# Optimization experiments

Measured on AMD Instinct MI355X. Metric: run time of the kernel, lower is better.

## Reference

```python
import jax, jax.numpy as jnp
import numpy as np

B, IN, H, OUT, E = 8192, 1024, 4096, 1024, 8
HG = H // 2  # gating hidden

def setup_inputs() -> dict:
    key = jax.random.key(0)
    ks = jax.random.split(key, 9)
    s_in = 1.0 / np.sqrt(IN)
    s_h = 1.0 / np.sqrt(H)
    s_hg = 1.0 / np.sqrt(HG)
    return {
        "x": jax.random.normal(ks[0], (B, IN), jnp.float32),
        # gating MLP: Linear(IN,HG) -> ReLU -> Linear(HG,E) -> softmax
        "gw1": jax.random.uniform(ks[1], (IN, HG), jnp.float32, -s_in, s_in),
        "gb1": jax.random.uniform(ks[2], (HG,), jnp.float32, -s_in, s_in),
        "gw2": jax.random.uniform(ks[3], (HG, E), jnp.float32, -s_hg, s_hg),
        "gb2": jax.random.uniform(ks[4], (E,), jnp.float32, -s_hg, s_hg),
        # experts: E x (Linear(IN,H) -> ReLU -> Linear(H,OUT))
        "ew1": jax.random.uniform(ks[5], (E, IN, H), jnp.float32, -s_in, s_in),
        "eb1": jax.random.uniform(ks[6], (E, H), jnp.float32, -s_in, s_in),
        "ew2": jax.random.uniform(ks[7], (E, H, OUT), jnp.float32, -s_h, s_h),
        "eb2": jax.random.uniform(ks[8], (E, OUT), jnp.float32, -s_h, s_h),
    }

def reference(x, gw1, gb1, gw2, gb2, ew1, eb1, ew2, eb2):
    # Gating network (dropout is a no-op in eval)
    gh = jax.nn.relu(x @ gw1 + gb1)                       # [B, HG]
    gates = jax.nn.softmax(gh @ gw2 + gb2, axis=1)        # [B, E]
    # All experts run on the full batch
    h = jax.nn.relu(jnp.einsum('bi,eih->beh', x, ew1) + eb1[None])  # [B, E, H]
    eo = jnp.einsum('beh,eho->beo', h, ew2) + eb2[None]             # [B, E, OUT]
    # Gate-weighted combine: (stacked * gates[...,None]).sum(dim=1)
    combined = jnp.einsum('beo,be->bo', eo, gates)        # [B, OUT]
    return combined
```

## Files before the change

### kernel.cpp

```cpp
#include <hip/hip_runtime.h>


#define DI __device__ __forceinline__

typedef _Float16 f16;
typedef _Float16 f16x8 __attribute__((ext_vector_type(8)));
typedef float f32x4 __attribute__((ext_vector_type(4)));

constexpr int BSZ  = 8192;
constexpr int IND  = 1024;
constexpr int HID  = 4096;
constexpr int OUTD = 1024;
constexpr int NE   = 8;
constexpr int HGD  = 2048;

__global__ __launch_bounds__(256) void conv_f32_f16_kernel(
    const float* __restrict__ in, f16* __restrict__ out)
{
    size_t i = ((size_t)blockIdx.x * 256 + threadIdx.x) * 8;
    const float4* p = (const float4*)(in + i);
    float4 a = p[0], b = p[1];
    f16x8 v = {(f16)a.x, (f16)a.y, (f16)a.z, (f16)a.w,
               (f16)b.x, (f16)b.y, (f16)b.z, (f16)b.w};
    *(f16x8*)(out + i) = v;
}

__global__ __launch_bounds__(256) void transpose_f32_f16_kernel(
    const float* __restrict__ W, f16* __restrict__ Wt, int K, int N)
{
    __shared__ float t[64][65];
    int n0 = blockIdx.x * 64, k0 = blockIdx.y * 64;
    int tx = threadIdx.x & 63, ty = threadIdx.x >> 6;
#pragma unroll
    for (int i = 0; i < 16; i++) {
        int k = i * 4 + ty;
        t[k][tx] = W[(size_t)(k0 + k) * N + n0 + tx];
    }
    __syncthreads();
#pragma unroll
    for (int i = 0; i < 16; i++) {
        int n = i * 4 + ty;
        Wt[(size_t)(n0 + n) * K + k0 + tx] = (f16)t[tx][n];
    }
}

DI void gload_lds16(const void* g, void* l)
{
    typedef const __attribute__((address_space(1))) unsigned int as1_t;
    typedef __attribute__((address_space(3))) unsigned int as3_t;
    __builtin_amdgcn_global_load_lds(
        (as1_t*)(unsigned long long)(__SIZE_TYPE__)g,
        (as3_t*)(unsigned int)(__SIZE_TYPE__)l,
        16, 0, 0);
}

template <bool RELU, bool GATE, bool OUT_F16, bool ACCUM>
__global__ __launch_bounds__(256, 2) void gemm_f16_kernel(
    const f16* __restrict__ A, const f16* __restrict__ Bt,
    const float* __restrict__ bias, const float* __restrict__ gate,
    void* __restrict__ Cptr, int M, int N, int K)
{
    constexpr int BK = 64;
    __shared__ __align__(16) f16 sA[128 * BK];
    __shared__ __align__(16) f16 sB[128 * BK];
    const int tid  = threadIdx.x;
    const int wid  = tid >> 6, lane = tid & 63;
    const size_t bm = (size_t)blockIdx.y * 128;
    const size_t bn = (size_t)blockIdx.x * 128;

    f32x4 acc[4][4] = {};

    int rr[4], oo[4];
#pragma unroll
    for (int i = 0; i < 4; i++) {
        int c = wid * 4 + i;
        rr[i] = c * 8 + (lane >> 3);
        oo[i] = ((((lane & 7) * 16) ^ ((rr[i] & 7) << 4)) >> 1);
    }
    const f16* Abase = A + bm * (size_t)K;
    const f16* Bbase = Bt + bn * (size_t)K;

    for (int kt = 0; kt < K; kt += BK) {
        __syncthreads();
#pragma unroll
        for (int i = 0; i < 4; i++) {
            int c = wid * 4 + i;
            gload_lds16(Abase + (size_t)rr[i] * K + kt + oo[i], (char*)sA + c * 1024);
            gload_lds16(Bbase + (size_t)rr[i] * K + kt + oo[i], (char*)sB + c * 1024);
        }
        __syncthreads();

#pragma unroll
        for (int kk = 0; kk < BK; kk += 32) {
            f16x8 av[4], bv[4];
            const int kb = (kk + ((lane >> 4) * 8)) * 2;
#pragma unroll
            for (int f = 0; f < 4; f++) {
                int Ra = ((wid >> 1) * 64) + f * 16 + (lane & 15);
                int Rb = ((wid & 1) * 64) + f * 16 + (lane & 15);
                av[f] = *(const f16x8*)((const char*)sA + Ra * 128 + (kb ^ ((Ra & 7) << 4)));
                bv[f] = *(const f16x8*)((const char*)sB + Rb * 128 + (kb ^ ((Rb & 7) << 4)));
            }
#pragma unroll
            for (int fm = 0; fm < 4; fm++)
#pragma unroll
                for (int fn = 0; fn < 4; fn++)
                    acc[fm][fn] = __builtin_amdgcn_mfma_f32_16x16x32_f16(
                        av[fm], bv[fn], acc[fm][fn], 0, 0, 0);
        }
    }

    const int wm = (wid >> 1) * 64, wn = (wid & 1) * 64;
    const int c0 = lane & 15, r0 = (lane >> 4) * 4;
#pragma unroll
    for (int fm = 0; fm < 4; fm++) {
#pragma unroll
        for (int r = 0; r < 4; r++) {
            const size_t row = bm + wm + fm * 16 + r0 + r;
            float g = 1.0f;
            if constexpr (GATE) g = gate[row * NE];
#pragma unroll
            for (int fn = 0; fn < 4; fn++) {
                const size_t col = bn + wn + fn * 16 + c0;
                float v = acc[fm][fn][r] + bias[col];
                if constexpr (RELU) v = fmaxf(v, 0.0f);
                if constexpr (GATE) v *= g;
                if constexpr (OUT_F16) {
                    ((f16*)Cptr)[row * (size_t)N + col] = (f16)v;
                } else {
                    float* p = (float*)Cptr + row * (size_t)N + col;
                    *p = ACCUM ? (*p + v) : v;
                }
            }
        }
    }
}

__global__ __launch_bounds__(256) void gate_softmax_kernel(
    const f16* __restrict__ gh, const float* __restrict__ gw2,
    const float* __restrict__ gb2, float* __restrict__ gates)
{
    const int row  = blockIdx.x * 4 + (threadIdx.x >> 6);
    const int lane = threadIdx.x & 63;
    const f16* r = gh + (size_t)row * HGD;
    float acc[NE] = {};
    for (int k = lane; k < HGD; k += 64) {
        float h = (float)r[k];
        const float* w = gw2 + (size_t)k * NE;
#pragma unroll
        for (int e = 0; e < NE; e++) acc[e] = fmaf(h, w[e], acc[e]);
    }
#pragma unroll
    for (int off = 32; off > 0; off >>= 1)
#pragma unroll
        for (int e = 0; e < NE; e++) acc[e] += __shfl_down(acc[e], off, 64);
    if (lane == 0) {
        float l[NE], m = -1e30f;
#pragma unroll
        for (int e = 0; e < NE; e++) { l[e] = acc[e] + gb2[e]; m = fmaxf(m, l[e]); }
        float s = 0.f;
#pragma unroll
        for (int e = 0; e < NE; e++) { l[e] = expf(l[e] - m); s += l[e]; }
        float inv = 1.0f / s;
#pragma unroll
        for (int e = 0; e < NE; e++) gates[(size_t)row * NE + e] = l[e] * inv;
    }
}

extern "C" void kernel_launch(void* const* d_in, const int* in_sizes, int n_in,
                              void* d_out, int out_size, void* d_ws, size_t ws_size,
                              hipStream_t stream)
{
    const float* x   = (const float*)d_in[0];
    const float* gw1 = (const float*)d_in[1];
    const float* gb1 = (const float*)d_in[2];
    const float* gw2 = (const float*)d_in[3];
    const float* gb2 = (const float*)d_in[4];
    const float* ew1 = (const float*)d_in[5];
    const float* eb1 = (const float*)d_in[6];
    const float* ew2 = (const float*)d_in[7];
    const float* eb2 = (const float*)d_in[8];
    float* out = (float*)d_out;

    char* ws = (char*)d_ws;
    float* gates = (float*)ws;
    f16* x16  = (f16*)(ws + (256 << 10));
    f16* wbuf = x16 + (size_t)BSZ * IND;
    f16* hbuf = wbuf + (size_t)HID * IND;
    f16* gh   = hbuf;

    conv_f32_f16_kernel<<<(BSZ * IND) / (256 * 8), 256, 0, stream>>>(x, x16);

    transpose_f32_f16_kernel<<<dim3(HGD / 64, IND / 64), 256, 0, stream>>>(gw1, wbuf, IND, HGD);
    gemm_f16_kernel<true, false, true, false>
        <<<dim3(HGD / 128, BSZ / 128), 256, 0, stream>>>(
            x16, wbuf, gb1, nullptr, gh, BSZ, HGD, IND);

    gate_softmax_kernel<<<BSZ / 4, 256, 0, stream>>>(gh, gw2, gb2, gates);

    for (int e = 0; e < NE; e++) {
        transpose_f32_f16_kernel<<<dim3(HID / 64, IND / 64), 256, 0, stream>>>(
            ew1 + (size_t)e * IND * HID, wbuf, IND, HID);
        gemm_f16_kernel<true, false, true, false>
            <<<dim3(HID / 128, BSZ / 128), 256, 0, stream>>>(
                x16, wbuf, eb1 + (size_t)e * HID, nullptr, hbuf, BSZ, HID, IND);

        transpose_f32_f16_kernel<<<dim3(OUTD / 64, HID / 64), 256, 0, stream>>>(
            ew2 + (size_t)e * HID * OUTD, wbuf, HID, OUTD);
        if (e == 0)
            gemm_f16_kernel<false, true, false, false>
                <<<dim3(OUTD / 128, BSZ / 128), 256, 0, stream>>>(
                    hbuf, wbuf, eb2 + (size_t)e * OUTD, gates + e, out, BSZ, OUTD, HID);
        else
            gemm_f16_kernel<false, true, false, true>
                <<<dim3(OUTD / 128, BSZ / 128), 256, 0, stream>>>(
                    hbuf, wbuf, eb2 + (size_t)e * OUTD, gates + e, out, BSZ, OUTD, HID);
    }
}
```

Baseline: 1.489 ms.

## Replace GEMM with 8-wave double-buffered ping-pong pipelined kernel using larger tiles

Replaces the simple 128x128 single-buffered f16 MFMA GEMM with a 512-thread kernel that uses 256xBN tiles, double-buffered LDS, B fragments held in registers, and explicit phase scheduling. Global-to-LDS loads for the next tile are interleaved with MFMA phases using barriers, waitcnt, and setprio. Workgroup IDs are remapped in an XCD-aware way. The goal is to hide memory latency and raise MFMA utilization, at the cost of much higher register and LDS pressure and fragile hand-tuned synchronization.

```diff
diff --git a/kernel.cpp b/kernel.cpp
--- a/kernel.cpp
+++ b/kernel.cpp
@@ -54,75 +54,141 @@
         16, 0, 0);
 }
 
-template <bool RELU, bool GATE, bool OUT_F16, bool ACCUM>
-__global__ __launch_bounds__(256, 2) void gemm_f16_kernel(
+
+#define PH(BUF, MH, KS, PRE, STAGE, VM)                                        \
+  {                                                                            \
+    f16x8 av0 = ldA(BUF, 0, MH, KS);                                           \
+    f16x8 av1 = ldA(BUF, 1, MH, KS);                                           \
+    f16x8 av2 = ldA(BUF, 2, MH, KS);                                           \
+    f16x8 av3 = ldA(BUF, 3, MH, KS);                                           \
+    if constexpr ((PRE) >= 0) {                                                \
+      _Pragma("unroll")                                                        \
+      for (int n = 0; n < NF; n++) breg[n][KS] = ldB(BUF, n, KS);              \
+    }                                                                          \
+    STAGE                                                                      \
+    __builtin_amdgcn_sched_barrier(0);                                         \
+    __builtin_amdgcn_s_barrier();                                              \
+    asm volatile("s_waitcnt lgkmcnt(0)" ::: "memory");                         \
+    __builtin_amdgcn_sched_barrier(0);                                         \
+    __builtin_amdgcn_s_setprio(1);                                             \
+    _Pragma("unroll")                                                          \
+    for (int n = 0; n < NF; n++) {                                             \
+      acc[(MH)*4+0][n] = __builtin_amdgcn_mfma_f32_16x16x32_f16(av0, breg[n][KS], acc[(MH)*4+0][n], 0, 0, 0); \
+      acc[(MH)*4+1][n] = __builtin_amdgcn_mfma_f32_16x16x32_f16(av1, breg[n][KS], acc[(MH)*4+1][n], 0, 0, 0); \
+      acc[(MH)*4+2][n] = __builtin_amdgcn_mfma_f32_16x16x32_f16(av2, breg[n][KS], acc[(MH)*4+2][n], 0, 0, 0); \
+      acc[(MH)*4+3][n] = __builtin_amdgcn_mfma_f32_16x16x32_f16(av3, breg[n][KS], acc[(MH)*4+3][n], 0, 0, 0); \
+    }                                                                          \
+    __builtin_amdgcn_s_setprio(0);                                             \
+    VM                                                                         \
+    __builtin_amdgcn_sched_barrier(0);                                         \
+    __builtin_amdgcn_s_barrier();                                              \
+    asm volatile("" ::: "memory");                                             \
+  }
+
+#define VMSTEP                                                                 \
+  { if (i + 1 == NI) { asm volatile("s_waitcnt vmcnt(0)"); }                   \
+    else if constexpr (BN == 256) { asm volatile("s_waitcnt vmcnt(4)"); }      \
+    else { asm volatile("s_waitcnt vmcnt(2)"); } }
+
+template <int BN, bool RELU, bool GATE, bool OUT_F16, bool ACCUM>
+__global__ __launch_bounds__(512, 2) void gemm8p_kernel(
     const f16* __restrict__ A, const f16* __restrict__ Bt,
     const float* __restrict__ bias, const float* __restrict__ gate,
     void* __restrict__ Cptr, int M, int N, int K)
 {
-    constexpr int BK = 64;
-    __shared__ __align__(16) f16 sA[128 * BK];
-    __shared__ __align__(16) f16 sB[128 * BK];
-    const int tid  = threadIdx.x;
-    const int wid  = tid >> 6, lane = tid & 63;
-    const size_t bm = (size_t)blockIdx.y * 128;
-    const size_t bn = (size_t)blockIdx.x * 128;
-
-    f32x4 acc[4][4] = {};
-
-    int rr[4], oo[4];
-#pragma unroll
-    for (int i = 0; i < 4; i++) {
-        int c = wid * 4 + i;
-        rr[i] = c * 8 + (lane >> 3);
-        oo[i] = ((((lane & 7) * 16) ^ ((rr[i] & 7) << 4)) >> 1);
-    }
-    const f16* Abase = A + bm * (size_t)K;
-    const f16* Bbase = Bt + bn * (size_t)K;
-
-    for (int kt = 0; kt < K; kt += BK) {
-        __syncthreads();
-#pragma unroll
-        for (int i = 0; i < 4; i++) {
-            int c = wid * 4 + i;
-            gload_lds16(Abase + (size_t)rr[i] * K + kt + oo[i], (char*)sA + c * 1024);
-            gload_lds16(Bbase + (size_t)rr[i] * K + kt + oo[i], (char*)sB + c * 1024);
-        }
-        __syncthreads();
-
-#pragma unroll
-        for (int kk = 0; kk < BK; kk += 32) {
-            f16x8 av[4], bv[4];
-            const int kb = (kk + ((lane >> 4) * 8)) * 2;
-#pragma unroll
-            for (int f = 0; f < 4; f++) {
-                int Ra = ((wid >> 1) * 64) + f * 16 + (lane & 15);
-                int Rb = ((wid & 1) * 64) + f * 16 + (lane & 15);
-                av[f] = *(const f16x8*)((const char*)sA + Ra * 128 + (kb ^ ((Ra & 7) << 4)));
-                bv[f] = *(const f16x8*)((const char*)sB + Rb * 128 + (kb ^ ((Rb & 7) << 4)));
-            }
-#pragma unroll
-            for (int fm = 0; fm < 4; fm++)
-#pragma unroll
-                for (int fn = 0; fn < 4; fn++)
-                    acc[fm][fn] = __builtin_amdgcn_mfma_f32_16x16x32_f16(
-                        av[fm], bv[fn], acc[fm][fn], 0, 0, 0);
-        }
-    }
-
-    const int wm = (wid >> 1) * 64, wn = (wid & 1) * 64;
+    constexpr int BM = 256, BK = 64;
+    constexpr int NF  = BN / 64;
+    constexpr int NBC = (BN * BK * 2) / 8192;
+    __shared__ __align__(16) f16 sA[2][BM * BK];
+    __shared__ __align__(16) f16 sB[2][BN * BK];
+
+    const int tid = threadIdx.x, wid = tid >> 6, lane = tid & 63;
+    const int wm = wid >> 2, wn = wid & 3;
+
+    const int nwg = gridDim.x;
+    const int bid = blockIdx.x;
+    const int wg  = (bid & 7) * (nwg >> 3) + (bid >> 3);
+    const int gx  = N / BN;
+    const size_t bm = (size_t)(wg / gx) * BM;
+    const size_t bn = (size_t)(wg % gx) * BN;
+
+    f32x4 acc[8][NF] = {};
+    f16x8 breg[NF][2];
+
+    const int srow = (wid << 3) + (lane >> 3);
+    const int scol = ((((lane & 7) << 4) ^ (((lane >> 3) & 7) << 4)) >> 1);
+    const f16* Ab = A  + (bm + srow) * (size_t)K + scol;
+    const f16* Bb = Bt + (bn + srow) * (size_t)K + scol;
+    char* sAb = (char*)&sA[0][0] + wid * 1024;
+    char* sBb = (char*)&sB[0][0] + wid * 1024;
+
+    auto stA = [&](int b, int q, int t) {
+        gload_lds16(Ab + (size_t)q * 64 * K + t * BK,
+                    sAb + b * (BM * BK * 2) + q * 8192);
+    };
+    auto stB = [&](int b, int q, int t) {
+        gload_lds16(Bb + (size_t)q * 64 * K + t * BK,
+                    sBb + b * (BN * BK * 2) + q * 8192);
+    };
+    auto ldA = [&](int b, int f, int mh, int ks) -> f16x8 {
+        int r  = wm * 128 + mh * 64 + f * 16 + (lane & 15);
+        int kb = (((ks * 32) + ((lane >> 4) << 3)) << 1) ^ ((r & 7) << 4);
+        return *(const f16x8*)((const char*)&sA[b][0] + r * 128 + kb);
+    };
+    auto ldB = [&](int b, int n, int ks) -> f16x8 {
+        int r  = wn * (BN / 4) + n * 16 + (lane & 15);
+        int kb = (((ks * 32) + ((lane >> 4) << 3)) << 1) ^ ((r & 7) << 4);
+        return *(const f16x8*)((const char*)&sB[b][0] + r * 128 + kb);
+    };
+
+    const int NT = K / BK, NI = NT / 2;
+
+#pragma unroll
+    for (int q = 0; q < 4; q++) stA(0, q, 0);
+#pragma unroll
+    for (int q = 0; q < NBC; q++) stB(0, q, 0);
+#pragma unroll
+    for (int q = 0; q < NBC; q++) stB(1, q, 1);
+    if constexpr (NBC == 4) { asm volatile("s_waitcnt vmcnt(4)"); }
+    else                    { asm volatile("s_waitcnt vmcnt(2)"); }
+    __builtin_amdgcn_s_barrier();
+    asm volatile("" ::: "memory");
+
+    for (int i = 0; i < NI; ++i) {
+        const int t = 2 * i;
+        const bool pf = (i + 1 < NI);
+        PH(0, 0, 0, 0,
+           { stA(1,0,t+1); stA(1,1,t+1); stA(1,2,t+1); stA(1,3,t+1); }, {})
+        PH(0, 0, 1, 1, {}, {})
+        PH(0, 1, 0, -1,
+           { if (pf) { stB(0,0,t+2); stB(0,1,t+2); } }, {})
+        PH(0, 1, 1, -1,
+           { if (pf) { if constexpr (NBC == 4) { stB(0,2,t+2); stB(0,3,t+2); } } },
+           VMSTEP)
+        PH(1, 0, 0, 0,
+           { if (pf) { stA(0,0,t+2); stA(0,1,t+2); stA(0,2,t+2); stA(0,3,t+2); } }, {})
+        PH(1, 0, 1, 1, {}, {})
+        PH(1, 1, 0, -1,
+           { if (pf) { stB(1,0,t+3); stB(1,1,t+3); } }, {})
+        PH(1, 1, 1, -1,
+           { if (pf) { if constexpr (NBC == 4) { stB(1,2,t+3); stB(1,3,t+3); } } },
+           VMSTEP)
+    }
+
+    const size_t row0 = bm + (size_t)wm * 128;
+    const int col0 = (int)bn + wn * (BN / 4);
     const int c0 = lane & 15, r0 = (lane >> 4) * 4;
 #pragma unroll
-    for (int fm = 0; fm < 4; fm++) {
+    for (int fm = 0; fm < 8; fm++) {
 #pragma unroll
         for (int r = 0; r < 4; r++) {
-            const size_t row = bm + wm + fm * 16 + r0 + r;
+            const size_t row = row0 + fm * 16 + r0 + r;
             float g = 1.0f;
             if constexpr (GATE) g = gate[row * NE];
 #pragma unroll
-            for (int fn = 0; fn < 4; fn++) {
-                const size_t col = bn + wn + fn * 16 + c0;
-                float v = acc[fm][fn][r] + bias[col];
+            for (int n = 0; n < NF; n++) {
+                const size_t col = (size_t)col0 + n * 16 + c0;
+                float v = acc[fm][n][r] + bias[col];
                 if constexpr (RELU) v = fmaxf(v, 0.0f);
                 if constexpr (GATE) v *= g;
                 if constexpr (OUT_F16) {
@@ -192,8 +258,8 @@
     conv_f32_f16_kernel<<<(BSZ * IND) / (256 * 8), 256, 0, stream>>>(x, x16);
 
     transpose_f32_f16_kernel<<<dim3(HGD / 64, IND / 64), 256, 0, stream>>>(gw1, wbuf, IND, HGD);
-    gemm_f16_kernel<true, false, true, false>
-        <<<dim3(HGD / 128, BSZ / 128), 256, 0, stream>>>(
+    gemm8p_kernel<256, true, false, true, false>
+        <<<(HGD / 256) * (BSZ / 256), 512, 0, stream>>>(
             x16, wbuf, gb1, nullptr, gh, BSZ, HGD, IND);
 
     gate_softmax_kernel<<<BSZ / 4, 256, 0, stream>>>(gh, gw2, gb2, gates);
@@ -201,19 +267,19 @@
     for (int e = 0; e < NE; e++) {
         transpose_f32_f16_kernel<<<dim3(HID / 64, IND / 64), 256, 0, stream>>>(
             ew1 + (size_t)e * IND * HID, wbuf, IND, HID);
-        gemm_f16_kernel<true, false, true, false>
-            <<<dim3(HID / 128, BSZ / 128), 256, 0, stream>>>(
+        gemm8p_kernel<256, true, false, true, false>
+            <<<(HID / 256) * (BSZ / 256), 512, 0, stream>>>(
                 x16, wbuf, eb1 + (size_t)e * HID, nullptr, hbuf, BSZ, HID, IND);
 
         transpose_f32_f16_kernel<<<dim3(OUTD / 64, HID / 64), 256, 0, stream>>>(
             ew2 + (size_t)e * HID * OUTD, wbuf, HID, OUTD);
         if (e == 0)
-            gemm_f16_kernel<false, true, false, false>
-                <<<dim3(OUTD / 128, BSZ / 128), 256, 0, stream>>>(
+            gemm8p_kernel<128, false, true, false, false>
+                <<<(OUTD / 128) * (BSZ / 256), 512, 0, stream>>>(
                     hbuf, wbuf, eb2 + (size_t)e * OUTD, gates + e, out, BSZ, OUTD, HID);
         else
-            gemm_f16_kernel<false, true, false, true>
-                <<<dim3(OUTD / 128, BSZ / 128), 256, 0, stream>>>(
+            gemm8p_kernel<128, false, true, false, true>
+                <<<(OUTD / 128) * (BSZ / 256), 512, 0, stream>>>(
                     hbuf, wbuf, eb2 + (size_t)e * OUTD, gates + e, out, BSZ, OUTD, HID);
     }
 }
```

After: 1.429 ms. 4.1% less time.
